# Optimization experiments

Hardware: AMD Instinct MI355X
Metric: run time of the kernel (lower is better)

Reference implementation:

```python
import jax, jax.numpy as jnp
import numpy as np

KERNEL_SIZE = 5


def setup_inputs() -> dict:
    key = jax.random.key(0)
    k1, k2, k3 = jax.random.split(key, 3)
    B, H, W = 32, 512, 512
    f = jax.random.uniform(k1, (B, H, W), dtype=jnp.float32)          # distribution function, non-negative
    K = jax.random.normal(k2, (KERNEL_SIZE, KERNEL_SIZE, H, W), dtype=jnp.float32) * 0.01  # per-pixel kernels
    dt = jax.random.uniform(k3, (B,), dtype=jnp.float32) * 0.1        # per-batch timestep
    return {"f": f, "K": K, "dt": dt}


def reference(f, K, dt):
    # f: (B,H,W); K: (k,k,H,W) position-dependent (unshared) kernels; dt: (B,)
    # Equivalent to: patches = unfold(pad(f)); df = einsum('bkv,kv->bv', patches, K.reshape(k*k,-1))
    # Implemented as a sum over the k*k kernel taps of shifted slices (avoids the
    # B*k^2*H*W patches tensor; loop is over the fixed kernel footprint, not data dims).
    k = K.shape[0]
    B, H, W = f.shape
    pl, pr = k // 2, (k - 1) // 2  # matches pad_size = (k//2, (k-1)//2)*2
    f_pad = jnp.pad(f, ((0, 0), (pl, pr), (pl, pr)))  # 'zeros' padding_mode
    df = jnp.zeros_like(f)
    for i in range(k):
        for j in range(k):
            df = df + f_pad[:, i:i + H, j:j + W] * K[i, j]
    out = f + df * dt[:, None, None]
    return jnp.maximum(out, 0.0)  # ensure_non_negative_f clamp
```

## Files before the change

### kernel.cpp

```cpp
#include <hip/hip_runtime.h>

#define H 512
#define W 512
#define HW (H * W)
#define BATCH 32
#define KS 5
#define NBH 8

typedef float nf2 __attribute__((ext_vector_type(2)));

__global__ __launch_bounds__(256, 1) void op2d_kernel(
    const float* __restrict__ f,
    const float* __restrict__ K,
    const float* __restrict__ dt,
    float* __restrict__ out)
{
    const int tid = threadIdx.x;
    const int c0  = tid * 2;
    const int r   = blockIdx.x;
    const int b0  = blockIdx.y * NBH;

    const bool wl = (c0 >= 2);
    const bool wr = (c0 <= 508);

    int rowoff[KS]; bool inb[KS];
#pragma unroll
    for (int i = 0; i < KS; ++i) {
        const int gr = r + i - 2;
        inb[i] = (gr >= 0) && (gr < H);
        rowoff[i] = (gr < 0 ? 0 : (gr >= H ? H - 1 : gr)) * W;
    }

    nf2 win[2][KS][3];
#define FROW(b, i, d) {                                                      \
        const float* fp = f + (size_t)(b0 + (b)) * HW + rowoff[i] + c0;      \
        (d)[0] = wl ? *(const nf2*)(fp - 2) : (nf2)0.f;                      \
        (d)[1] =      *(const nf2*)(fp);                                     \
        (d)[2] = wr ? *(const nf2*)(fp + 2) : (nf2)0.f;                      \
    }

#pragma unroll
    for (int i = 0; i < KS; ++i) FROW(0, i, win[0][i]);

    nf2 Kt[KS][KS];
#pragma unroll
    for (int i = 0; i < KS; ++i) {
#pragma unroll
        for (int j = 0; j < KS; ++j)
            Kt[i][j] = inb[i]
                ? *(const nf2*)(K + (size_t)(i * KS + j) * HW
                                  + (size_t)r * W + c0)
                : (nf2)0.f;
    }

#pragma unroll
    for (int b = 0; b < NBH; ++b) {
        if (b + 1 < NBH) {
#pragma unroll
            for (int i = 0; i < KS; ++i) FROW(b + 1, i, win[(b + 1) & 1][i]);
        }

        const float dtv = dt[b0 + b];

        float ax = 0.f, ay = 0.f;
#pragma unroll
        for (int i = 0; i < KS; ++i) {
            const nf2 e0 = win[b & 1][i][0];
            const nf2 e1 = win[b & 1][i][1];
            const nf2 e2 = win[b & 1][i][2];
            const float w[6] = { e0.x, e0.y, e1.x, e1.y, e2.x, e2.y };
#pragma unroll
            for (int j = 0; j < KS; ++j) {
                ax += Kt[i][j].x * w[j];
                ay += Kt[i][j].y * w[j + 1];
            }
        }

        const nf2 fc = win[b & 1][2][1];
        nf2 o;
        o.x = fmaxf(fc.x + ax * dtv, 0.f);
        o.y = fmaxf(fc.y + ay * dtv, 0.f);
        __builtin_nontemporal_store(o,
            (nf2*)(out + ((size_t)(b0 + b) * H + r) * W + c0));
    }
#undef FROW
}

extern "C" void kernel_launch(void* const* d_in, const int* in_sizes, int n_in,
                              void* d_out, int out_size, void* d_ws, size_t ws_size,
                              hipStream_t stream) {
    const float* f  = (const float*)d_in[0];
    const float* K  = (const float*)d_in[1];
    const float* dt = (const float*)d_in[2];
    float* out = (float*)d_out;

    dim3 block(256);
    dim3 grid(H, BATCH / NBH);
    op2d_kernel<<<grid, block, 0, stream>>>(f, K, dt, out);
}
```

Baseline: 137.3 us.

## Stage f rows in LDS via async global_load_lds with double buffering

Each thread used to load overlapping left, center and right float2 windows for all five rows straight into registers. Now each block copies the five input rows per batch into a double-buffered shared-memory tile using direct global-to-LDS loads, and every thread reads its stencil window from LDS. The block-to-row mapping is also swizzled so that consecutively launched blocks work on rows spread across the image. The aim is to cut redundant global and L1 traffic and register pressure. In exchange it adds a block barrier per batch step, and correctness depends on the barrier waiting for the async LDS loads to finish.

```diff
diff --git a/kernel.cpp b/kernel.cpp
--- a/kernel.cpp
+++ b/kernel.cpp
@@ -1,4 +1,5 @@
 #include <hip/hip_runtime.h>
+#include <stdint.h>
 
 #define H 512
 #define W 512
@@ -6,8 +7,11 @@
 #define BATCH 32
 #define KS 5
 #define NBH 8
+#define WPAD 516
 
 typedef float nf2 __attribute__((ext_vector_type(2)));
+typedef __attribute__((address_space(3))) uint32_t lds_u32;
+typedef const __attribute__((address_space(1))) uint32_t glb_u32;
 
 __global__ __launch_bounds__(256, 1) void op2d_kernel(
     const float* __restrict__ f,
@@ -15,13 +19,19 @@
     const float* __restrict__ dt,
     float* __restrict__ out)
 {
-    const int tid = threadIdx.x;
-    const int c0  = tid * 2;
-    const int r   = blockIdx.x;
-    const int b0  = blockIdx.y * NBH;
+    __shared__ float fl[2][KS][WPAD];
+
+    const int tid  = threadIdx.x;
+    const int c0   = tid * 2;
+    const int lane = tid & 63;
+    const int wv   = tid >> 6;
+    const int bx   = blockIdx.x;
+    const int r    = (bx & 7) * 64 + (bx >> 3);
+    const int b0   = blockIdx.y * NBH;
 
     const bool wl = (c0 >= 2);
     const bool wr = (c0 <= 508);
+    const int  cl = wl ? c0 - 2 : 0;
 
     int rowoff[KS]; bool inb[KS];
 #pragma unroll
@@ -31,43 +41,49 @@
         rowoff[i] = (gr < 0 ? 0 : (gr >= H ? H - 1 : gr)) * W;
     }
 
-    nf2 win[2][KS][3];
-#define FROW(b, i, d) {                                                      \
-        const float* fp = f + (size_t)(b0 + (b)) * HW + rowoff[i] + c0;      \
-        (d)[0] = wl ? *(const nf2*)(fp - 2) : (nf2)0.f;                      \
-        (d)[1] =      *(const nf2*)(fp);                                     \
-        (d)[2] = wr ? *(const nf2*)(fp + 2) : (nf2)0.f;                      \
+#define STAGE(b, buf) {                                                      \
+        _Pragma("unroll")                                                    \
+        for (int c = 0; c < 10; ++c) {                                       \
+            if ((c & 3) == wv) {                                             \
+                const int row = c >> 1, half = c & 1;                        \
+                const float* g = f + (size_t)(b0 + (b)) * HW                 \
+                                   + rowoff[row] + half * 256 + lane * 4;    \
+                __builtin_amdgcn_global_load_lds((glb_u32*)g,                \
+                    (lds_u32*)&fl[buf][row][half * 256], 16, 0, 0);          \
+            }                                                                \
+        }                                                                    \
     }
 
-#pragma unroll
-    for (int i = 0; i < KS; ++i) FROW(0, i, win[0][i]);
+    STAGE(0, 0);
 
     nf2 Kt[KS][KS];
 #pragma unroll
-    for (int i = 0; i < KS; ++i) {
+    for (int i = 0; i < KS; ++i)
 #pragma unroll
         for (int j = 0; j < KS; ++j)
             Kt[i][j] = inb[i]
                 ? *(const nf2*)(K + (size_t)(i * KS + j) * HW
                                   + (size_t)r * W + c0)
                 : (nf2)0.f;
-    }
+
+    __syncthreads();
 
 #pragma unroll
     for (int b = 0; b < NBH; ++b) {
-        if (b + 1 < NBH) {
-#pragma unroll
-            for (int i = 0; i < KS; ++i) FROW(b + 1, i, win[(b + 1) & 1][i]);
-        }
+        if (b + 1 < NBH) STAGE(b + 1, (b + 1) & 1);
 
         const float dtv = dt[b0 + b];
 
         float ax = 0.f, ay = 0.f;
+        nf2 fc;
 #pragma unroll
         for (int i = 0; i < KS; ++i) {
-            const nf2 e0 = win[b & 1][i][0];
-            const nf2 e1 = win[b & 1][i][1];
-            const nf2 e2 = win[b & 1][i][2];
+            nf2 e0 = *(const nf2*)&fl[b & 1][i][cl];
+            nf2 e1 = *(const nf2*)&fl[b & 1][i][c0];
+            nf2 e2 = *(const nf2*)&fl[b & 1][i][c0 + 2];
+            e0 = wl ? e0 : (nf2)0.f;
+            e2 = wr ? e2 : (nf2)0.f;
+            if (i == 2) fc = e1;
             const float w[6] = { e0.x, e0.y, e1.x, e1.y, e2.x, e2.y };
 #pragma unroll
             for (int j = 0; j < KS; ++j) {
@@ -76,14 +92,15 @@
             }
         }
 
-        const nf2 fc = win[b & 1][2][1];
         nf2 o;
         o.x = fmaxf(fc.x + ax * dtv, 0.f);
         o.y = fmaxf(fc.y + ay * dtv, 0.f);
         __builtin_nontemporal_store(o,
             (nf2*)(out + ((size_t)(b0 + b) * H + r) * W + c0));
+
+        if (b + 1 < NBH) __syncthreads();
     }
-#undef FROW
+#undef STAGE
 }
 
 extern "C" void kernel_launch(void* const* d_in, const int* in_sizes, int n_in,
```

Result: faster. 116.8 us (-15.0%).
